# Performance work log

Hardware: AMD Instinct MI355X
Metric: run time of the kernel (lower is better)

The kernel has to match this reference:

```python
import jax, jax.numpy as jnp
import numpy as np

B, S, K, H = 8192, 512, 8, 512  # batch, size_half, n_segments, hidden
EPS = 1e-6


def setup_inputs() -> dict:
    key = jax.random.key(0)
    k0, k1, k2, k3 = jax.random.split(key, 4)
    x_input = jax.random.uniform(k0, (B, 2 * S), dtype=jnp.float32)  # in [0,1)
    log_density = jax.random.normal(k1, (B, 1), dtype=jnp.float32)
    W1 = jax.random.normal(k2, (S, H), dtype=jnp.float32) / np.sqrt(S).astype(np.float32)
    b1 = jnp.zeros((H,), jnp.float32)
    W2 = jax.random.normal(k3, (H, S * (2 * K + 1)), dtype=jnp.float32) / np.sqrt(H).astype(np.float32)
    b2 = jnp.zeros((S * (2 * K + 1),), jnp.float32)
    return {"x_input": x_input, "log_density": log_density,
            "W1": W1, "b1": b1, "W2": W2, "b2": b2}


def reference(x_input, log_density, W1, b1, W2, b2):
    # even_sites=True: passive half a = first S cols, transformed half b = last S
    x_a = x_input[:, :S]
    x_b = x_input[:, S:]

    # NeuralNetwork: Linear -> tanh -> Linear -> tanh (final_activation == activation)
    hid = jnp.tanh((x_a - 0.5) @ W1 + b1)
    net = jnp.tanh(hid @ W2 + b2).reshape(-1, S, 2 * K + 1)  # [B,S,2K+1]
    h_raw, w_raw = net[..., :K + 1], net[..., K + 1:]

    w_norm = jax.nn.softmax(w_raw, axis=2)                       # [B,S,K]
    eh = jnp.exp(h_raw)                                          # [B,S,K+1]
    h_norm = eh / jnp.sum(0.5 * w_norm * (eh[..., :-1] + eh[..., 1:]),
                          axis=2, keepdims=True)

    b = x_a.shape[0]
    x_knots = jnp.concatenate(
        [jnp.full((b, S, 1), -EPS, x_a.dtype), jnp.cumsum(w_norm, axis=2)], axis=2)  # [B,S,K+1]
    pdf_area = 0.5 * w_norm * (h_norm[..., :-1] + h_norm[..., 1:])
    phi_knots = jnp.concatenate(
        [jnp.zeros((b, S, 1), x_a.dtype), jnp.cumsum(pdf_area, axis=2)], axis=2)     # [B,S,K+1]

    # searchsorted(left) - 1 == (# knots strictly below x) - 1
    k_ind = jnp.clip(jnp.sum(x_knots < x_b[..., None], axis=2) - 1, 0, K - 1)[..., None]

    w_k = jnp.take_along_axis(w_norm, k_ind, axis=2)
    h_k = jnp.take_along_axis(h_norm, k_ind, axis=2)
    h_kp1 = jnp.take_along_axis(h_norm, k_ind + 1, axis=2)
    x_km1 = jnp.take_along_axis(x_knots, k_ind, axis=2)
    phi_km1 = jnp.take_along_axis(phi_knots, k_ind, axis=2)

    alpha = (x_b[..., None] - x_km1) / w_k
    phi_b = (phi_km1 + alpha * h_k * w_k
             + 0.5 * alpha ** 2 * (h_kp1 - h_k) * w_k)[..., 0]    # [B,S]

    phi_out = jnp.concatenate([x_a, phi_b], axis=1)               # [B,2S]
    new_log_density = log_density - jnp.sum(
        jnp.log(h_k + alpha * (h_kp1 - h_k)), axis=1)             # [B,1]
    return phi_out, new_log_density
```

## Files before the change

### kernel.cpp

```cpp
#include <hip/hip_runtime.h>
#include <stdint.h>
#include <math.h>

#define BROWS 8192
#define SDIM  512
#define HDIM  512
#define NCOL  8704
#define EPSK  1e-6f
#define LOG2E  1.442695041f
#define TWOL2E 2.885390082f
#define LN2    0.6931471806f

typedef __attribute__((ext_vector_type(8))) short bf16x8;
typedef __attribute__((ext_vector_type(4))) short bf16x4;
typedef __attribute__((ext_vector_type(4))) float f32x4;

__device__ __forceinline__ unsigned short f2bf(float f) {
    unsigned u = __float_as_uint(f);
    u += 0x7fffu + ((u >> 16) & 1u);
    return (unsigned short)(u >> 16);
}
__device__ __forceinline__ unsigned short f2bf_fast(float f) {
    return (unsigned short)((__float_as_uint(f) + 0x8000u) >> 16);
}
__device__ __forceinline__ float bf2f(unsigned short s) {
    return __uint_as_float(((unsigned)s) << 16);
}
#define EXP2F(x) __builtin_amdgcn_exp2f(x)
#define LOG2F(x) __builtin_amdgcn_logf(x)
#define RCPF(x)  __builtin_amdgcn_rcpf(x)

__device__ __forceinline__ float ftanh(float x) {
    float e = EXP2F(TWOL2E * x);
    return (e - 1.f) * RCPF(e + 1.f);
}
__device__ __forceinline__ float ftanh_l2e(float acc, float bias2L) {
    float e = EXP2F(fmaf(acc, TWOL2E, bias2L));
    return fmaf(e, LOG2E, -LOG2E) * RCPF(e + 1.f);
}

#define GLD16(g, l)                                                         \
    __builtin_amdgcn_global_load_lds(                                       \
        (const __attribute__((address_space(1))) void*)(g),                 \
        (__attribute__((address_space(3))) void*)(l), 16, 0, 0)

__global__ __launch_bounds__(256) void prep_a(
    const float* __restrict__ W1, unsigned short* __restrict__ W1T,
    const float* __restrict__ logd, float* __restrict__ out)
{
    __shared__ float tile[32 * 33];
    const int t   = threadIdx.x;
    const int bid = blockIdx.x;
    if (bid < 256) {
        const int cb = (bid & 15) * 32;
        const int rb = (bid >> 4) * 32;
        const int ty = t >> 3, tx = (t & 7) * 4;
        float4 v = *(const float4*)&W1[(size_t)(rb + ty) * HDIM + cb + tx];
        tile[ty * 33 + tx + 0] = v.x;
        tile[ty * 33 + tx + 1] = v.y;
        tile[ty * 33 + tx + 2] = v.z;
        tile[ty * 33 + tx + 3] = v.w;
        __syncthreads();
        const int oy = t >> 3, ox = (t & 7) * 4;
        bf16x4 o;
        o[0] = (short)f2bf(tile[(ox + 0) * 33 + oy]);
        o[1] = (short)f2bf(tile[(ox + 1) * 33 + oy]);
        o[2] = (short)f2bf(tile[(ox + 2) * 33 + oy]);
        o[3] = (short)f2bf(tile[(ox + 3) * 33 + oy]);
        *(bf16x4*)&W1T[(size_t)(cb + oy) * SDIM + rb + ox] = o;
    } else {
        const int b = (bid - 256) * 256 + t;
        out[(size_t)BROWS * (2 * SDIM) + b] = logd[b];
    }
}

__global__ __launch_bounds__(256) void mega_k(
    const float* __restrict__ x,
    const unsigned short* __restrict__ W1T,
    const float* __restrict__ b1,
    unsigned short* __restrict__ hid,
    const float* __restrict__ W2,
    unsigned short* __restrict__ W2p,
    float* __restrict__ out)
{
    __shared__ float Asf[2][64 * 32];
    __shared__ short Bsb[2][128 * 32];
    const int bid = blockIdx.x;
    const int tid = threadIdx.x;

    if (bid < 512) {
        const int flat = bid;
        const int xcd  = flat & 7;
        const int j8   = flat >> 3;
        const int bn   = (j8 & 3) * 128;
        const int bm   = (xcd * 16 + (j8 >> 2)) * 64;

        const int lane = tid & 63;
        const int wave = tid >> 6;
        const int ln15 = lane & 15;
        const int quad = lane >> 4;
        const int wm   = (wave >> 1) * 32;
        const int wn   = (wave & 1) * 64;
        const int brow = lane >> 2;
        const int bsub_sw = (lane & 3) ^ ((lane >> 3) & 3);
        const int arow8   = lane >> 3;
        const int aslot_sw = (lane & 7) ^ (arow8 & 7);
        const int qsw = (quad ^ ((ln15 >> 1) & 3)) * 8;
        const int ag  = ln15 & 7;

        f32x4 acc[2][4];
#pragma unroll
        for (int i = 0; i < 2; i++)
#pragma unroll
            for (int j = 0; j < 4; j++) acc[i][j] = (f32x4){0.f, 0.f, 0.f, 0.f};

        const float* asrc = &x[(size_t)(bm + arow8) * (2 * SDIM) + aslot_sw * 4];
        const unsigned short* bsrc = &W1T[(size_t)(bn + brow) * SDIM + bsub_sw * 8];

        auto issue = [&](int n, int p) {
#pragma unroll
            for (int c = 0; c < 2; ++c) {
                const int ca = wave * 2 + c;
                GLD16(asrc + (size_t)ca * 8 * (2 * SDIM) + n * 32, &Asf[p][ca * 256]);
            }
#pragma unroll
            for (int c = 0; c < 2; ++c) {
                const int cb = wave * 2 + c;
                GLD16(bsrc + (size_t)cb * 16 * SDIM + n * 32, &Bsb[p][cb * 512]);
            }
        };

        issue(0, 0);
        for (int n = 0; n < 16; ++n) {
            __syncthreads();
            if (n < 15) issue(n + 1, (n + 1) & 1);
            const float* As = Asf[n & 1];
            const short* Bs = Bsb[n & 1];

            bf16x8 af[2], bfr[4];
#pragma unroll
            for (int i = 0; i < 2; ++i) {
                const int r = wm + i * 16 + ln15;
                f32x4 a0 = *(const f32x4*)&As[r * 32 + ((2 * quad + 0) ^ ag) * 4];
                f32x4 a1 = *(const f32x4*)&As[r * 32 + ((2 * quad + 1) ^ ag) * 4];
                bf16x8 v;
                v[0] = (short)f2bf_fast(a0[0] - 0.5f); v[1] = (short)f2bf_fast(a0[1] - 0.5f);
                v[2] = (short)f2bf_fast(a0[2] - 0.5f); v[3] = (short)f2bf_fast(a0[3] - 0.5f);
                v[4] = (short)f2bf_fast(a1[0] - 0.5f); v[5] = (short)f2bf_fast(a1[1] - 0.5f);
                v[6] = (short)f2bf_fast(a1[2] - 0.5f); v[7] = (short)f2bf_fast(a1[3] - 0.5f);
                af[i] = v;
            }
#pragma unroll
            for (int j = 0; j < 4; ++j)
                bfr[j] = *(const bf16x8*)&Bsb[n & 1][(wn + j * 16 + ln15) * 32 + qsw];
#pragma unroll
            for (int i = 0; i < 2; ++i)
#pragma unroll
                for (int j = 0; j < 4; ++j)
                    acc[i][j] = __builtin_amdgcn_mfma_f32_16x16x32_bf16(af[i], bfr[j], acc[i][j], 0, 0, 0);
            (void)Bs; (void)As;
        }

#pragma unroll
        for (int j = 0; j < 4; j++) {
            const int col = bn + wn + j * 16 + ln15;
            const float bias = b1[col];
#pragma unroll
            for (int i = 0; i < 2; i++) {
#pragma unroll
                for (int r = 0; r < 4; r++) {
                    const int row = bm + wm + i * 16 + quad * 4 + r;
                    hid[(size_t)row * HDIM + col] = f2bf(ftanh(acc[i][j][r] + bias));
                }
            }
        }
    } else if (bid < 2688) {
        float* tile = &Asf[0][0];
        const int ct = (bid - 512) >> 2;
        const int kq = (bid - 512) & 3;
        const int colbase = ct * 16;
        const int colblk = ct / 17;
        const int chunk  = ct - colblk * 17;
        const int k32 = tid >> 3;
        const int c2  = (tid & 7) * 2;
        const int r   = tid >> 4;
        const int e2  = (tid & 15) * 2;
        for (int kk = kq * 4; kk < kq * 4 + 4; ++kk) {
            float2 v = *(const float2*)&W2[(size_t)(kk * 32 + k32) * NCOL + colbase + c2];
            __syncthreads();
            tile[k32 * 17 + c2 + 0] = v.x;
            tile[k32 * 17 + c2 + 1] = v.y;
            __syncthreads();
            const size_t off = (((size_t)colblk * 16 + kk) * 17 + chunk) * 512;
            ushort2 o;
            o.x = f2bf(tile[(e2 + 0) * 17 + r]);
            o.y = f2bf(tile[(e2 + 1) * 17 + r]);
            *(ushort2*)&W2p[off + (size_t)r * 32 + e2] = o;
        }
    } else {
        const int bt = bid - 2688;
        const float4* xi = (const float4*)x;
        float4* oo = (float4*)out;
        const int base = bt * 4096 + tid;
#pragma unroll
        for (int k2 = 0; k2 < 16; ++k2) {
            const int f = base + k2 * 256;
            const int row = f >> 7, c4 = f & 127;
            oo[(size_t)row * 256 + c4] = xi[(size_t)row * 256 + c4];
        }
    }
}

__global__ __launch_bounds__(256, 2) void gemm2_spline_mfma(
    const unsigned short* __restrict__ hid,
    const unsigned short* __restrict__ W2p,
    const float* __restrict__ b2,
    const float* __restrict__ x,
    float* __restrict__ out)
{
    __shared__ short smem[35904];

    const int bm     = blockIdx.x * 128;
    const int colblk = blockIdx.y;
    const int tid  = threadIdx.x;
    const int lane = tid & 63;
    const int wave = tid >> 6;
    const int ln15 = lane & 15;
    const int quad = lane >> 4;
    const int brow = lane >> 2;
    const int bsub_sw = (lane & 3) ^ ((lane >> 3) & 3);
    const int qsw = (quad ^ ((ln15 >> 1) & 3)) * 8;
    const int jstart = wave * 4;
    const int jcount = (wave == 3) ? 5 : 4;
    const int bcol = colblk * 272;

    f32x4 acc[8][5];
#pragma unroll
    for (int i = 0; i < 8; i++)
#pragma unroll
        for (int j = 0; j < 5; j++) acc[i][j] = (f32x4){0.f, 0.f, 0.f, 0.f};

    const unsigned short* bbase =
        W2p + ((size_t)colblk * 16) * 17 * 512 + (size_t)(lane >> 2) * 32 + (size_t)bsub_sw * 8;
    const unsigned short* abase0 =
        &hid[(size_t)(bm + wave * 32 + brow) * HDIM + bsub_sw * 8];
    const unsigned short* abase1 = abase0 + 16 * HDIM;

    auto issue = [&](int n, int p) {
        short* dst = smem + p * 12800;
        GLD16(abase0 + n * 32, &dst[(2 * wave + 0) * 512]);
        GLD16(abase1 + n * 32, &dst[(2 * wave + 1) * 512]);
        const unsigned short* bk = bbase + (size_t)n * (17 * 512);
        for (int c = 0; c < jcount; ++c) {
            const int chunk = jstart + c;
            GLD16(bk + (size_t)chunk * 512, &dst[4096 + chunk * 512]);
        }
    };

    issue(0, 0);
    for (int n = 0; n < 16; ++n) {
        __syncthreads();
        if (n < 15) issue(n + 1, (n + 1) & 1);
        const short* As = smem + (n & 1) * 12800;
        const short* Bs = As + 4096;

        bf16x8 bfr[5];
        if (wave == 3) {
#pragma unroll
            for (int j = 0; j < 5; ++j)
                bfr[j] = *(const bf16x8*)&Bs[((jstart + j) * 16 + ln15) * 32 + qsw];
        } else {
#pragma unroll
            for (int j = 0; j < 4; ++j)
                bfr[j] = *(const bf16x8*)&Bs[((jstart + j) * 16 + ln15) * 32 + qsw];
        }

        __builtin_amdgcn_s_setprio(1);
#define ILOOP(JC)                                                               \
        _Pragma("unroll") for (int i = 0; i < 8; ++i) {                         \
            bf16x8 af = *(const bf16x8*)&As[(i * 16 + ln15) * 32 + qsw];        \
            _Pragma("unroll") for (int j = 0; j < (JC); ++j)                    \
                acc[i][j] = __builtin_amdgcn_mfma_f32_16x16x32_bf16(af, bfr[j], acc[i][j], 0, 0, 0); \
        }
        if (wave == 3) { ILOOP(5) } else { ILOOP(4) }
#undef ILOOP
        __builtin_amdgcn_s_setprio(0);
    }

    const int sp = tid & 15;
    const int r0 = tid >> 4;
    const int sglob = colblk * 16 + sp;
    float xbv[8];
#pragma unroll
    for (int t = 0; t < 8; ++t)
        xbv[t] = x[(size_t)(bm + t * 16 + r0) * (2 * SDIM) + SDIM + sglob];
    float b2v[5];
#pragma unroll
    for (int j = 0; j < 5; ++j)
        b2v[j] = b2[bcol + (jstart + j) * 16 + ln15] * TWOL2E;

    __syncthreads();
#define EPI1(JC)                                                                \
    _Pragma("unroll") for (int j = 0; j < (JC); ++j) {                          \
        const int col_l = (jstart + j) * 16 + ln15;                             \
        const float bias2L = b2v[j];                                            \
        _Pragma("unroll") for (int i = 0; i < 8; ++i) {                         \
            bf16x4 o;                                                           \
            _Pragma("unroll") for (int r = 0; r < 4; ++r)                       \
                o[r] = (short)f2bf_fast(ftanh_l2e(acc[i][j][r], bias2L));       \
            *(bf16x4*)&smem[col_l * 132 + i * 16 + quad * 4] = o;               \
        }                                                                       \
    }
    if (wave == 3) { EPI1(5) } else { EPI1(4) }
#undef EPI1
    __syncthreads();

    for (int t = 0; t < 8; ++t) {
        const int row_l = t * 16 + r0;
        const int row = bm + row_l;
        const int cbase = sp * 17 * 132 + row_l;

        float s[17];
#pragma unroll
        for (int c = 0; c < 17; c++)
            s[c] = bf2f((unsigned short)smem[cbase + c * 132]);

        float eh[9], e[8];
#pragma unroll
        for (int j = 0; j < 9; j++) eh[j] = EXP2F(s[j]);
#pragma unroll
        for (int c = 0; c < 8; c++) e[c]  = EXP2F(s[9 + c]);

        float cum_e[8], cum_u[8];
        cum_e[0] = e[0];
        cum_u[0] = e[0] * (eh[0] + eh[1]);
#pragma unroll
        for (int c = 1; c < 8; c++) {
            cum_e[c] = cum_e[c - 1] + e[c];
            cum_u[c] = fmaf(e[c], eh[c] + eh[c + 1], cum_u[c - 1]);
        }
        const float se = cum_e[7];
        const float su = cum_u[7];
        const float thr = xbv[t] * se;

        float selE = e[0], selEH = eh[0], selEH1 = eh[1];
        float selCE = -EPSK * se, selCU = 0.f;
#pragma unroll
        for (int c = 1; c < 8; c++) {
            const bool tt = (cum_e[c - 1] < thr);
            selE   = tt ? e[c]         : selE;
            selEH  = tt ? eh[c]        : selEH;
            selEH1 = tt ? eh[c + 1]    : selEH1;
            selCE  = tt ? cum_e[c - 1] : selCE;
            selCU  = tt ? cum_u[c - 1] : selCU;
        }

        const float alpha = (thr - selCE) * RCPF(selE);
        const float dlt   = selEH1 - selEH;
        const float su_inv = RCPF(su);
        float p = fmaf(2.f * alpha, selE * selEH, selCU);
        p = fmaf(alpha * alpha, selE * dlt, p);
        out[(size_t)row * (2 * SDIM) + SDIM + sglob] = p * su_inv;

        const float g = fmaf(alpha, dlt, selEH) * (2.f * se * su_inv);
        float lg = LOG2F(g);
        lg += __shfl_xor(lg, 1);
        lg += __shfl_xor(lg, 2);
        lg += __shfl_xor(lg, 4);
        lg += __shfl_xor(lg, 8);
        if (sp == 0)
            atomicAdd(&out[(size_t)BROWS * (2 * SDIM) + row], -lg * LN2);
    }
}

extern "C" void kernel_launch(void* const* d_in, const int* in_sizes, int n_in,
                              void* d_out, int out_size, void* d_ws, size_t ws_size,
                              hipStream_t stream) {
    const float* x    = (const float*)d_in[0];
    const float* logd = (const float*)d_in[1];
    const float* W1   = (const float*)d_in[2];
    const float* b1   = (const float*)d_in[3];
    const float* W2   = (const float*)d_in[4];
    const float* b2   = (const float*)d_in[5];
    float* out = (float*)d_out;

    char* ws = (char*)d_ws;
    unsigned short* W1T = (unsigned short*)(ws + 32768);
    unsigned short* W2p = (unsigned short*)(ws + 557056);
    unsigned short* hid = (unsigned short*)(ws + 9469952);

    prep_a<<<288, 256, 0, stream>>>(W1, W1T, logd, out);
    mega_k<<<2944, 256, 0, stream>>>(x, W1T, b1, hid, W2, W2p, out);
    gemm2_spline_mfma<<<dim3(64, 32), 256, 0, stream>>>(hid, W2p, b2, x, out);
}
```

Baseline: 224.0 us.

## Fuse three launches into one persistent cooperative kernel with grid syncs

Merges the three separate kernels (W1 transpose/logd copy, GEMM1 plus W2 packing plus x copy, GEMM2 plus spline) into one persistent cooperative kernel. Blocks loop over work units, with grid.sync between the phases. The aim is to remove kernel launch gaps and tail effects between stages. In exchange, W2 packing can no longer overlap with GEMM1, the grid is fixed at 256 or 512 blocks, and every phase must run under the 2-blocks-per-CU launch bounds and the larger shared memory footprint. The old three-kernel path stays as a fallback if the cooperative launch fails.

```diff
diff --git a/kernel.cpp b/kernel.cpp
--- a/kernel.cpp
+++ b/kernel.cpp
@@ -1,6 +1,9 @@
 #include <hip/hip_runtime.h>
+#include <hip/hip_cooperative_groups.h>
 #include <stdint.h>
 #include <math.h>
+
+namespace cg = cooperative_groups;
 
 #define BROWS 8192
 #define SDIM  512
@@ -44,185 +47,180 @@
         (const __attribute__((address_space(1))) void*)(g),                 \
         (__attribute__((address_space(3))) void*)(l), 16, 0, 0)
 
-__global__ __launch_bounds__(256) void prep_a(
-    const float* __restrict__ W1, unsigned short* __restrict__ W1T,
-    const float* __restrict__ logd, float* __restrict__ out)
-{
-    __shared__ float tile[32 * 33];
-    const int t   = threadIdx.x;
-    const int bid = blockIdx.x;
-    if (bid < 256) {
-        const int cb = (bid & 15) * 32;
-        const int rb = (bid >> 4) * 32;
-        const int ty = t >> 3, tx = (t & 7) * 4;
-        float4 v = *(const float4*)&W1[(size_t)(rb + ty) * HDIM + cb + tx];
-        tile[ty * 33 + tx + 0] = v.x;
-        tile[ty * 33 + tx + 1] = v.y;
-        tile[ty * 33 + tx + 2] = v.z;
-        tile[ty * 33 + tx + 3] = v.w;
+
+__device__ __forceinline__ void do_w1t_unit(
+    int u, int t, const float* __restrict__ W1,
+    unsigned short* __restrict__ W1T, short* smem)
+{
+    float* tile = (float*)smem;
+    __syncthreads();
+    const int cb = (u & 15) * 32;
+    const int rb = (u >> 4) * 32;
+    const int ty = t >> 3, tx = (t & 7) * 4;
+    float4 v = *(const float4*)&W1[(size_t)(rb + ty) * HDIM + cb + tx];
+    tile[ty * 33 + tx + 0] = v.x;
+    tile[ty * 33 + tx + 1] = v.y;
+    tile[ty * 33 + tx + 2] = v.z;
+    tile[ty * 33 + tx + 3] = v.w;
+    __syncthreads();
+    const int oy = t >> 3, ox = (t & 7) * 4;
+    bf16x4 o;
+    o[0] = (short)f2bf(tile[(ox + 0) * 33 + oy]);
+    o[1] = (short)f2bf(tile[(ox + 1) * 33 + oy]);
+    o[2] = (short)f2bf(tile[(ox + 2) * 33 + oy]);
+    o[3] = (short)f2bf(tile[(ox + 3) * 33 + oy]);
+    *(bf16x4*)&W1T[(size_t)(cb + oy) * SDIM + rb + ox] = o;
+}
+
+__device__ __forceinline__ void do_logd_unit(
+    int u, int t, const float* __restrict__ logd, float* __restrict__ out)
+{
+    const int b = u * 256 + t;
+    out[(size_t)BROWS * (2 * SDIM) + b] = logd[b];
+}
+
+__device__ __forceinline__ void do_pack_unit(
+    int u, int t, const float* __restrict__ W2,
+    unsigned short* __restrict__ W2p, short* smem)
+{
+    float* tile = (float*)smem;
+    const int ct = u >> 2;
+    const int kq = u & 3;
+    const int colbase = ct * 16;
+    const int colblk = ct / 17;
+    const int chunk  = ct - colblk * 17;
+    const int k32 = t >> 3;
+    const int c2  = (t & 7) * 2;
+    const int r   = t >> 4;
+    const int e2  = (t & 15) * 2;
+    for (int kk = kq * 4; kk < kq * 4 + 4; ++kk) {
+        float2 v = *(const float2*)&W2[(size_t)(kk * 32 + k32) * NCOL + colbase + c2];
         __syncthreads();
-        const int oy = t >> 3, ox = (t & 7) * 4;
-        bf16x4 o;
-        o[0] = (short)f2bf(tile[(ox + 0) * 33 + oy]);
-        o[1] = (short)f2bf(tile[(ox + 1) * 33 + oy]);
-        o[2] = (short)f2bf(tile[(ox + 2) * 33 + oy]);
-        o[3] = (short)f2bf(tile[(ox + 3) * 33 + oy]);
-        *(bf16x4*)&W1T[(size_t)(cb + oy) * SDIM + rb + ox] = o;
-    } else {
-        const int b = (bid - 256) * 256 + t;
-        out[(size_t)BROWS * (2 * SDIM) + b] = logd[b];
-    }
-}
-
-__global__ __launch_bounds__(256) void mega_k(
-    const float* __restrict__ x,
-    const unsigned short* __restrict__ W1T,
-    const float* __restrict__ b1,
-    unsigned short* __restrict__ hid,
-    const float* __restrict__ W2,
-    unsigned short* __restrict__ W2p,
-    float* __restrict__ out)
-{
-    __shared__ float Asf[2][64 * 32];
-    __shared__ short Bsb[2][128 * 32];
-    const int bid = blockIdx.x;
-    const int tid = threadIdx.x;
-
-    if (bid < 512) {
-        const int flat = bid;
-        const int xcd  = flat & 7;
-        const int j8   = flat >> 3;
-        const int bn   = (j8 & 3) * 128;
-        const int bm   = (xcd * 16 + (j8 >> 2)) * 64;
-
-        const int lane = tid & 63;
-        const int wave = tid >> 6;
-        const int ln15 = lane & 15;
-        const int quad = lane >> 4;
-        const int wm   = (wave >> 1) * 32;
-        const int wn   = (wave & 1) * 64;
-        const int brow = lane >> 2;
-        const int bsub_sw = (lane & 3) ^ ((lane >> 3) & 3);
-        const int arow8   = lane >> 3;
-        const int aslot_sw = (lane & 7) ^ (arow8 & 7);
-        const int qsw = (quad ^ ((ln15 >> 1) & 3)) * 8;
-        const int ag  = ln15 & 7;
-
-        f32x4 acc[2][4];
-#pragma unroll
-        for (int i = 0; i < 2; i++)
-#pragma unroll
-            for (int j = 0; j < 4; j++) acc[i][j] = (f32x4){0.f, 0.f, 0.f, 0.f};
-
-        const float* asrc = &x[(size_t)(bm + arow8) * (2 * SDIM) + aslot_sw * 4];
-        const unsigned short* bsrc = &W1T[(size_t)(bn + brow) * SDIM + bsub_sw * 8];
-
-        auto issue = [&](int n, int p) {
-#pragma unroll
-            for (int c = 0; c < 2; ++c) {
-                const int ca = wave * 2 + c;
-                GLD16(asrc + (size_t)ca * 8 * (2 * SDIM) + n * 32, &Asf[p][ca * 256]);
+        tile[k32 * 17 + c2 + 0] = v.x;
+        tile[k32 * 17 + c2 + 1] = v.y;
+        __syncthreads();
+        const size_t off = (((size_t)colblk * 16 + kk) * 17 + chunk) * 512;
+        ushort2 o;
+        o.x = f2bf(tile[(e2 + 0) * 17 + r]);
+        o.y = f2bf(tile[(e2 + 1) * 17 + r]);
+        *(ushort2*)&W2p[off + (size_t)r * 32 + e2] = o;
+    }
+}
+
+__device__ __forceinline__ void do_copy_unit(
+    int u, int t, const float* __restrict__ x, float* __restrict__ out)
+{
+    const float4* xi = (const float4*)x;
+    float4* oo = (float4*)out;
+    const int base = u * 4096 + t;
+#pragma unroll
+    for (int k2 = 0; k2 < 16; ++k2) {
+        const int f = base + k2 * 256;
+        const int row = f >> 7, c4 = f & 127;
+        oo[(size_t)row * 256 + c4] = xi[(size_t)row * 256 + c4];
+    }
+}
+
+__device__ __forceinline__ void gemm1_tile(
+    int flat, int tid, const float* __restrict__ x,
+    const unsigned short* __restrict__ W1T, const float* __restrict__ b1,
+    unsigned short* __restrict__ hid, short* smem)
+{
+    __syncthreads();
+    const int xcd  = flat & 7;
+    const int j8   = flat >> 3;
+    const int bn   = (j8 & 3) * 128;
+    const int bm   = (xcd * 16 + (j8 >> 2)) * 64;
+
+    const int lane = tid & 63;
+    const int wave = tid >> 6;
+    const int ln15 = lane & 15;
+    const int quad = lane >> 4;
+    const int wm   = (wave >> 1) * 32;
+    const int wn   = (wave & 1) * 64;
+    const int brow = lane >> 2;
+    const int bsub_sw = (lane & 3) ^ ((lane >> 3) & 3);
+    const int arow8   = lane >> 3;
+    const int aslot_sw = (lane & 7) ^ (arow8 & 7);
+    const int qsw = (quad ^ ((ln15 >> 1) & 3)) * 8;
+    const int ag  = ln15 & 7;
+
+    f32x4 acc[2][4];
+#pragma unroll
+    for (int i = 0; i < 2; i++)
+#pragma unroll
+        for (int j = 0; j < 4; j++) acc[i][j] = (f32x4){0.f, 0.f, 0.f, 0.f};
+
+    const float* asrc = &x[(size_t)(bm + arow8) * (2 * SDIM) + aslot_sw * 4];
+    const unsigned short* bsrc = &W1T[(size_t)(bn + brow) * SDIM + bsub_sw * 8];
+    float* AsfB = (float*)smem;
+    short* BsbB = smem + 8192;
+
+    auto issue = [&](int n, int p) {
+#pragma unroll
+        for (int c = 0; c < 2; ++c) {
+            const int ca = wave * 2 + c;
+            GLD16(asrc + (size_t)ca * 8 * (2 * SDIM) + n * 32, &AsfB[p * 2048 + ca * 256]);
+        }
+#pragma unroll
+        for (int c = 0; c < 2; ++c) {
+            const int cb = wave * 2 + c;
+            GLD16(bsrc + (size_t)cb * 16 * SDIM + n * 32, &BsbB[p * 4096 + cb * 512]);
+        }
+    };
+
+    issue(0, 0);
+    for (int n = 0; n < 16; ++n) {
+        __syncthreads();
+        if (n < 15) issue(n + 1, (n + 1) & 1);
+        const float* As = AsfB + (n & 1) * 2048;
+        const short* Bs = BsbB + (n & 1) * 4096;
+
+        bf16x8 af[2], bfr[4];
+#pragma unroll
+        for (int i = 0; i < 2; ++i) {
+            const int r = wm + i * 16 + ln15;
+            f32x4 a0 = *(const f32x4*)&As[r * 32 + ((2 * quad + 0) ^ ag) * 4];
+            f32x4 a1 = *(const f32x4*)&As[r * 32 + ((2 * quad + 1) ^ ag) * 4];
+            bf16x8 v;
+            v[0] = (short)f2bf_fast(a0[0] - 0.5f); v[1] = (short)f2bf_fast(a0[1] - 0.5f);
+            v[2] = (short)f2bf_fast(a0[2] - 0.5f); v[3] = (short)f2bf_fast(a0[3] - 0.5f);
+            v[4] = (short)f2bf_fast(a1[0] - 0.5f); v[5] = (short)f2bf_fast(a1[1] - 0.5f);
+            v[6] = (short)f2bf_fast(a1[2] - 0.5f); v[7] = (short)f2bf_fast(a1[3] - 0.5f);
+            af[i] = v;
+        }
+#pragma unroll
+        for (int j = 0; j < 4; ++j)
+            bfr[j] = *(const bf16x8*)&Bs[(wn + j * 16 + ln15) * 32 + qsw];
+#pragma unroll
+        for (int i = 0; i < 2; ++i)
+#pragma unroll
+            for (int j = 0; j < 4; ++j)
+                acc[i][j] = __builtin_amdgcn_mfma_f32_16x16x32_bf16(af[i], bfr[j], acc[i][j], 0, 0, 0);
+    }
+
+#pragma unroll
+    for (int j = 0; j < 4; j++) {
+        const int col = bn + wn + j * 16 + ln15;
+        const float bias = b1[col];
+#pragma unroll
+        for (int i = 0; i < 2; i++) {
+#pragma unroll
+            for (int r = 0; r < 4; r++) {
+                const int row = bm + wm + i * 16 + quad * 4 + r;
+                hid[(size_t)row * HDIM + col] = f2bf(ftanh(acc[i][j][r] + bias));
             }
-#pragma unroll
-            for (int c = 0; c < 2; ++c) {
-                const int cb = wave * 2 + c;
-                GLD16(bsrc + (size_t)cb * 16 * SDIM + n * 32, &Bsb[p][cb * 512]);
-            }
-        };
-
-        issue(0, 0);
-        for (int n = 0; n < 16; ++n) {
-            __syncthreads();
-            if (n < 15) issue(n + 1, (n + 1) & 1);
-            const float* As = Asf[n & 1];
-            const short* Bs = Bsb[n & 1];
-
-            bf16x8 af[2], bfr[4];
-#pragma unroll
-            for (int i = 0; i < 2; ++i) {
-                const int r = wm + i * 16 + ln15;
-                f32x4 a0 = *(const f32x4*)&As[r * 32 + ((2 * quad + 0) ^ ag) * 4];
-                f32x4 a1 = *(const f32x4*)&As[r * 32 + ((2 * quad + 1) ^ ag) * 4];
-                bf16x8 v;
-                v[0] = (short)f2bf_fast(a0[0] - 0.5f); v[1] = (short)f2bf_fast(a0[1] - 0.5f);
-                v[2] = (short)f2bf_fast(a0[2] - 0.5f); v[3] = (short)f2bf_fast(a0[3] - 0.5f);
-                v[4] = (short)f2bf_fast(a1[0] - 0.5f); v[5] = (short)f2bf_fast(a1[1] - 0.5f);
-                v[6] = (short)f2bf_fast(a1[2] - 0.5f); v[7] = (short)f2bf_fast(a1[3] - 0.5f);
-                af[i] = v;
-            }
-#pragma unroll
-            for (int j = 0; j < 4; ++j)
-                bfr[j] = *(const bf16x8*)&Bsb[n & 1][(wn + j * 16 + ln15) * 32 + qsw];
-#pragma unroll
-            for (int i = 0; i < 2; ++i)
-#pragma unroll
-                for (int j = 0; j < 4; ++j)
-                    acc[i][j] = __builtin_amdgcn_mfma_f32_16x16x32_bf16(af[i], bfr[j], acc[i][j], 0, 0, 0);
-            (void)Bs; (void)As;
-        }
-
-#pragma unroll
-        for (int j = 0; j < 4; j++) {
-            const int col = bn + wn + j * 16 + ln15;
-            const float bias = b1[col];
-#pragma unroll
-            for (int i = 0; i < 2; i++) {
-#pragma unroll
-                for (int r = 0; r < 4; r++) {
-                    const int row = bm + wm + i * 16 + quad * 4 + r;
-                    hid[(size_t)row * HDIM + col] = f2bf(ftanh(acc[i][j][r] + bias));
-                }
-            }
-        }
-    } else if (bid < 2688) {
-        float* tile = &Asf[0][0];
-        const int ct = (bid - 512) >> 2;
-        const int kq = (bid - 512) & 3;
-        const int colbase = ct * 16;
-        const int colblk = ct / 17;
-        const int chunk  = ct - colblk * 17;
-        const int k32 = tid >> 3;
-        const int c2  = (tid & 7) * 2;
-        const int r   = tid >> 4;
-        const int e2  = (tid & 15) * 2;
-        for (int kk = kq * 4; kk < kq * 4 + 4; ++kk) {
-            float2 v = *(const float2*)&W2[(size_t)(kk * 32 + k32) * NCOL + colbase + c2];
-            __syncthreads();
-            tile[k32 * 17 + c2 + 0] = v.x;
-            tile[k32 * 17 + c2 + 1] = v.y;
-            __syncthreads();
-            const size_t off = (((size_t)colblk * 16 + kk) * 17 + chunk) * 512;
-            ushort2 o;
-            o.x = f2bf(tile[(e2 + 0) * 17 + r]);
-            o.y = f2bf(tile[(e2 + 1) * 17 + r]);
-            *(ushort2*)&W2p[off + (size_t)r * 32 + e2] = o;
-        }
-    } else {
-        const int bt = bid - 2688;
-        const float4* xi = (const float4*)x;
-        float4* oo = (float4*)out;
-        const int base = bt * 4096 + tid;
-#pragma unroll
-        for (int k2 = 0; k2 < 16; ++k2) {
-            const int f = base + k2 * 256;
-            const int row = f >> 7, c4 = f & 127;
-            oo[(size_t)row * 256 + c4] = xi[(size_t)row * 256 + c4];
-        }
-    }
-}
-
-__global__ __launch_bounds__(256, 2) void gemm2_spline_mfma(
-    const unsigned short* __restrict__ hid,
-    const unsigned short* __restrict__ W2p,
-    const float* __restrict__ b2,
-    const float* __restrict__ x,
-    float* __restrict__ out)
-{
-    __shared__ short smem[35904];
-
-    const int bm     = blockIdx.x * 128;
-    const int colblk = blockIdx.y;
-    const int tid  = threadIdx.x;
+        }
+    }
+}
+
+__device__ __forceinline__ void gemm2_tile(
+    int bm, int colblk, int tid,
+    const unsigned short* __restrict__ hid, const unsigned short* __restrict__ W2p,
+    const float* __restrict__ b2, const float* __restrict__ x,
+    float* __restrict__ out, short* smem)
+{
+    __syncthreads();
     const int lane = tid & 63;
     const int wave = tid >> 6;
     const int ln15 = lane & 15;
@@ -241,7 +239,7 @@
         for (int j = 0; j < 5; j++) acc[i][j] = (f32x4){0.f, 0.f, 0.f, 0.f};
 
     const unsigned short* bbase =
-        W2p + ((size_t)colblk * 16) * 17 * 512 + (size_t)(lane >> 2) * 32 + (size_t)bsub_sw * 8;
+        W2p + ((size_t)colblk * 16) * 17 * 512 + (size_t)brow * 32 + (size_t)bsub_sw * 8;
     const unsigned short* abase0 =
         &hid[(size_t)(bm + wave * 32 + brow) * HDIM + bsub_sw * 8];
     const unsigned short* abase1 = abase0 + 16 * HDIM;
@@ -373,6 +371,66 @@
     }
 }
 
+__global__ __launch_bounds__(256, 2) void fused_k(
+    const float* __restrict__ x, const float* __restrict__ logd,
+    const float* __restrict__ W1, const float* __restrict__ b1,
+    const float* __restrict__ W2, const float* __restrict__ b2,
+    unsigned short* __restrict__ W1T, unsigned short* __restrict__ W2p,
+    unsigned short* __restrict__ hid, float* __restrict__ out, int nb)
+{
+    __shared__ short smem[35904];
+    cg::grid_group grid = cg::this_grid();
+    const int tid = threadIdx.x;
+    const int bid = blockIdx.x;
+
+    for (int u = bid; u < 2720; u += nb) {
+        if (u < 256)        do_w1t_unit(u, tid, W1, W1T, smem);
+        else if (u < 288)   do_logd_unit(u - 256, tid, logd, out);
+        else if (u < 2464)  do_pack_unit(u - 288, tid, W2, W2p, smem);
+        else                do_copy_unit(u - 2464, tid, x, out);
+    }
+    grid.sync();
+    for (int t = bid; t < 512; t += nb)
+        gemm1_tile(t, tid, x, W1T, b1, hid, smem);
+    grid.sync();
+    for (int t = bid; t < 2048; t += nb) {
+        const int colblk = t & 31;
+        const int bm = (t >> 5) * 128;
+        gemm2_tile(bm, colblk, tid, hid, W2p, b2, x, out, smem);
+    }
+}
+
+__global__ __launch_bounds__(256) void prep_a_k(
+    const float* __restrict__ W1, unsigned short* __restrict__ W1T,
+    const float* __restrict__ logd, float* __restrict__ out)
+{
+    __shared__ short smem[2112];
+    if (blockIdx.x < 256) do_w1t_unit(blockIdx.x, threadIdx.x, W1, W1T, smem);
+    else                  do_logd_unit(blockIdx.x - 256, threadIdx.x, logd, out);
+}
+
+__global__ __launch_bounds__(256) void mega_k(
+    const float* __restrict__ x, const unsigned short* __restrict__ W1T,
+    const float* __restrict__ b1, unsigned short* __restrict__ hid,
+    const float* __restrict__ W2, unsigned short* __restrict__ W2p,
+    float* __restrict__ out)
+{
+    __shared__ short smem[16384];
+    const int bid = blockIdx.x;
+    if (bid < 512)        gemm1_tile(bid, threadIdx.x, x, W1T, b1, hid, smem);
+    else if (bid < 2688)  do_pack_unit(bid - 512, threadIdx.x, W2, W2p, smem);
+    else                  do_copy_unit(bid - 2688, threadIdx.x, x, out);
+}
+
+__global__ __launch_bounds__(256, 2) void gemm2_k(
+    const unsigned short* __restrict__ hid, const unsigned short* __restrict__ W2p,
+    const float* __restrict__ b2, const float* __restrict__ x,
+    float* __restrict__ out)
+{
+    __shared__ short smem[35904];
+    gemm2_tile(blockIdx.x * 128, blockIdx.y, threadIdx.x, hid, W2p, b2, x, out, smem);
+}
+
 extern "C" void kernel_launch(void* const* d_in, const int* in_sizes, int n_in,
                               void* d_out, int out_size, void* d_ws, size_t ws_size,
                               hipStream_t stream) {
@@ -389,7 +447,21 @@
     unsigned short* W2p = (unsigned short*)(ws + 557056);
     unsigned short* hid = (unsigned short*)(ws + 9469952);
 
-    prep_a<<<288, 256, 0, stream>>>(W1, W1T, logd, out);
-    mega_k<<<2944, 256, 0, stream>>>(x, W1T, b1, hid, W2, W2p, out);
-    gemm2_spline_mfma<<<dim3(64, 32), 256, 0, stream>>>(hid, W2p, b2, x, out);
-}
+    bool coop_ok = false;
+    int nbpc = 0;
+    hipError_t qerr = hipOccupancyMaxActiveBlocksPerMultiprocessor(&nbpc, fused_k, 256, 0);
+    if (qerr == hipSuccess && nbpc >= 1) {
+        int nb = (nbpc >= 2) ? 512 : 256;
+        void* args[] = {(void*)&x, (void*)&logd, (void*)&W1, (void*)&b1,
+                        (void*)&W2, (void*)&b2, (void*)&W1T, (void*)&W2p,
+                        (void*)&hid, (void*)&out, (void*)&nb};
+        hipError_t lerr = hipLaunchCooperativeKernel(
+            fused_k, dim3(nb), dim3(256), args, 0u, stream);
+        coop_ok = (lerr == hipSuccess);
+    }
+    if (!coop_ok) {
+        prep_a_k<<<288, 256, 0, stream>>>(W1, W1T, logd, out);
+        mega_k<<<2944, 256, 0, stream>>>(x, W1T, b1, hid, W2, W2p, out);
+        gemm2_k<<<dim3(64, 32), 256, 0, stream>>>(hid, W2p, b2, x, out);
+    }
+}
```

Result: slower. 373.5 us (+66.7%).
